# Kernel tuning notes

Hardware: AMD Instinct MI355X
Metric: run time of the kernel (lower is better)

The kernel has to match this reference:

```python
import jax, jax.numpy as jnp
import numpy as np

B, S = 32, 8192
HE, HD = 256, 256  # encoder_hidden_size, decoder_hidden_size


def setup_inputs() -> dict:
    key = jax.random.key(0)
    ks = jax.random.split(key, 8)
    scale = 1.0 / np.sqrt(HD)
    scale_e = 1.0 / np.sqrt(HE)
    return {
        "query": jax.random.normal(ks[0], (B, 1, HD), dtype=jnp.float32),
        "keys": jax.random.normal(ks[1], (B, S, HE), dtype=jnp.float32),
        "Wa_w": jax.random.uniform(ks[2], (HD, HD), jnp.float32, -scale, scale),
        "Wa_b": jax.random.uniform(ks[3], (HD,), jnp.float32, -scale, scale),
        "Ua_w": jax.random.uniform(ks[4], (HD, HE), jnp.float32, -scale_e, scale_e),
        "Ua_b": jax.random.uniform(ks[5], (HD,), jnp.float32, -scale_e, scale_e),
        "Va_w": jax.random.uniform(ks[6], (1, HD), jnp.float32, -scale, scale),
        "Va_b": jax.random.uniform(ks[7], (1,), jnp.float32, -scale, scale),
    }


def reference(query, keys, Wa_w, Wa_b, Ua_w, Ua_b, Va_w, Va_b):
    # q_proj: [B, 1, HD]; k_proj: [B, S, HD]
    q_proj = jnp.einsum("bqd,hd->bqh", query, Wa_w) + Wa_b
    k_proj = jnp.einsum("bse,he->bsh", keys, Ua_w) + Ua_b
    # scores: [B, S] -> [B, 1, S]
    scores = jnp.einsum("bsh,h->bs", jnp.tanh(q_proj + k_proj), Va_w[0]) + Va_b[0]
    weights = jax.nn.softmax(scores, axis=-1)[:, None, :]  # [B, 1, S]
    context = jnp.einsum("bqs,bse->bqe", weights, keys)    # [B, 1, HE]
    return (context, weights)
```

## Files before the change

kernel.cpp:

```cpp
#include <hip/hip_runtime.h>
#include <hip/hip_bf16.h>
#include <stdint.h>

#define B_ 32
#define S_ 8192
#define HD_ 256
#define HE_ 256
#define CHUNK 256
#define ROWS 16
#define MSTEPS (CHUNK/ROWS)
#define NCHUNK (S_/CHUNK)

typedef __attribute__((ext_vector_type(8))) short bf16x8;
typedef __attribute__((ext_vector_type(4))) float f32x4;

__device__ __forceinline__ uint32_t cvt_pk_bf16(float lo, float hi) {
  uint32_t r;
  asm("v_cvt_pk_bf16_f32 %0, %1, %2" : "=v"(r) : "v"(lo), "v"(hi));
  return r;
}
__device__ __forceinline__ float bf2f(unsigned short h) {
  return __uint_as_float(((uint32_t)h) << 16);
}
__device__ __forceinline__ float tanh_fast(float x) {
  float e = __expf(2.0f * x);
  return 1.0f - 2.0f * __builtin_amdgcn_rcpf(e + 1.0f);
}
template<int CTRL>
__device__ __forceinline__ float dpp_shr_add(float v) {
  int t = __builtin_amdgcn_update_dpp(0, __float_as_int(v), CTRL, 0xf, 0xf, true);
  return v + __int_as_float(t);
}
__device__ __forceinline__ float row16_sum(float v) {
  v = dpp_shr_add<0x118>(v);
  v = dpp_shr_add<0x114>(v);
  v = dpp_shr_add<0x112>(v);
  v = dpp_shr_add<0x111>(v);
  return v;
}

__global__ void prep_kernel(const float* __restrict__ query,
                            const float* __restrict__ Wa_w,
                            const float* __restrict__ Wa_b,
                            const float* __restrict__ Ua_w,
                            const float* __restrict__ Ua_b,
                            float* __restrict__ qv,
                            unsigned short* __restrict__ ua_bf) {
  const int blk = blockIdx.x, t = threadIdx.x;
  if (blk < B_) {
    __shared__ float qs[HD_];
    qs[t] = query[blk * HD_ + t];
    __syncthreads();
    const float* wr = Wa_w + (size_t)t * HD_;
    float s = Wa_b[t] + Ua_b[t];
#pragma unroll 8
    for (int d = 0; d < HD_; ++d) s += qs[d] * wr[d];
    qv[blk * HD_ + t] = s;
  } else {
    const int base = (blk - B_) * 2048 + t * 8;
    float4 v0 = *(const float4*)(Ua_w + base);
    float4 v1 = *(const float4*)(Ua_w + base + 4);
    uint4 pk;
    pk.x = cvt_pk_bf16(v0.x, v0.y);
    pk.y = cvt_pk_bf16(v0.z, v0.w);
    pk.z = cvt_pk_bf16(v1.x, v1.y);
    pk.w = cvt_pk_bf16(v1.z, v1.w);
    *(uint4*)(ua_bf + base) = pk;
  }
}

__global__ __launch_bounds__(512)
__attribute__((amdgpu_waves_per_eu(4, 4)))
void main_kernel(const float* __restrict__ keys,
                 const float* __restrict__ qv,
                 const float* __restrict__ Va_w,
                 const unsigned short* __restrict__ ua_bf,
                 float* __restrict__ wexp_g,
                 float* __restrict__ partials) {
  __shared__ __align__(16) char kt[2 * ROWS * 512];
  __shared__ float sc[ROWS][9];
  __shared__ float swp[ROWS];
  __shared__ float num2[512];

  const int t = threadIdx.x;
  const int b = blockIdx.y;
  const int chunk = blockIdx.x;
  const int s0 = chunk * CHUNK;
  const int lane = t & 63;
  const int w = t >> 6;
  const int ln = lane & 15;
  const int hi = lane >> 4;

  const unsigned short* ub0 = ua_bf + (size_t)(w * 32 + ln) * HE_ + hi * 8;
  const unsigned short* ub1 = ub0 + 16 * HE_;
  bf16x8 bb0[8], bb1[8];
#pragma unroll
  for (int k = 0; k < 8; ++k) {
    bb0[k] = *(const bf16x8*)(ub0 + k * 32);
    bb1[k] = *(const bf16x8*)(ub1 + k * 32);
  }
  const float q0  = qv[b * HD_ + w * 32 + ln];
  const float q1  = qv[b * HD_ + w * 32 + 16 + ln];
  const float va0 = Va_w[w * 32 + ln];
  const float va1 = Va_w[w * 32 + 16 + ln];

  const int srow = t >> 5;
  const int scch = t & 31;
  const float* ksrc = keys + ((size_t)b * S_ + s0 + srow) * HE_ + scch * 8;
  const int ldsoff = srow * 512 + ((scch * 16) ^ ((srow & 7) << 4));

  {
    float4 a0 = *(const float4*)(ksrc);
    float4 a1 = *(const float4*)(ksrc + 4);
    uint4 pk;
    pk.x = cvt_pk_bf16(a0.x, a0.y);
    pk.y = cvt_pk_bf16(a0.z, a0.w);
    pk.z = cvt_pk_bf16(a1.x, a1.y);
    pk.w = cvt_pk_bf16(a1.z, a1.w);
    *(uint4*)(kt + ldsoff) = pk;
  }
  __syncthreads();

  const int half = t >> 8;
  const int e2 = (t & 255) * 2;
  const int asw = (ln & 7) << 4;
  float num = 0.f;

  for (int i = 0; i < MSTEPS; ++i) {
    char* cur = kt + (i & 1) * (ROWS * 512);
    char* nxt = kt + ((i + 1) & 1) * (ROWS * 512);

    float4 ga0, ga1;
    if (i + 1 < MSTEPS) {
      const float* kA = ksrc + (size_t)(i + 1) * ROWS * HE_;
      ga0 = *(const float4*)(kA);
      ga1 = *(const float4*)(kA + 4);
    }

    f32x4 a00 = {0.f,0.f,0.f,0.f}, a01 = {0.f,0.f,0.f,0.f};
    const char* arow = cur + ln * 512;
#pragma unroll
    for (int k = 0; k < 8; ++k) {
      bf16x8 af = *(const bf16x8*)(arow + ((k * 64 + hi * 16) ^ asw));
      a00 = __builtin_amdgcn_mfma_f32_16x16x32_bf16(af, bb0[k], a00, 0, 0, 0);
      a01 = __builtin_amdgcn_mfma_f32_16x16x32_bf16(af, bb1[k], a01, 0, 0, 0);
    }

#pragma unroll
    for (int r = 0; r < 4; ++r) {
      float v = tanh_fast(a00[r] + q0) * va0 + tanh_fast(a01[r] + q1) * va1;
      v = row16_sum(v);
      if (ln == 15) sc[hi * 4 + r][w] = v;
    }
    __syncthreads();

    if (t < ROWS) {
      float s = sc[t][0];
#pragma unroll
      for (int ww = 1; ww < 8; ++ww) s += sc[t][ww];
      float e = __expf(s);
      swp[t] = e;
      wexp_g[(size_t)b * S_ + s0 + i * ROWS + t] = e;
    }
    __syncthreads();

#pragma unroll
    for (int rr = 0; rr < 8; ++rr) {
      const int row = half * 8 + rr;
      unsigned short kv = *(const unsigned short*)(cur + row * 512 + (e2 ^ ((row & 7) << 4)));
      num += swp[row] * bf2f(kv);
    }

    if (i + 1 < MSTEPS) {
      uint4 pk;
      pk.x = cvt_pk_bf16(ga0.x, ga0.y);
      pk.y = cvt_pk_bf16(ga0.z, ga0.w);
      pk.z = cvt_pk_bf16(ga1.x, ga1.y);
      pk.w = cvt_pk_bf16(ga1.z, ga1.w);
      *(uint4*)(nxt + ldsoff) = pk;
    }
    __syncthreads();
  }

  num2[t] = num;
  __syncthreads();
  if (t < 256) {
    partials[((size_t)b * NCHUNK + chunk) * 256 + t] = num2[t] + num2[t + 256];
  }
}

__global__ void combine_kernel(const float* __restrict__ wexp_g,
                               const float* __restrict__ partials,
                               float* __restrict__ out) {
  __shared__ float red[4];
  __shared__ float rdsh;
  const int b = blockIdx.x, t = threadIdx.x;
  const float* we = wexp_g + (size_t)b * S_;
  float s = 0.f;
#pragma unroll 4
  for (int i = t; i < S_; i += 256) s += we[i];
#pragma unroll
  for (int mm = 32; mm; mm >>= 1) s += __shfl_xor(s, mm, 64);
  if ((t & 63) == 0) red[t >> 6] = s;
  __syncthreads();
  if (t == 0) rdsh = 1.0f / (red[0] + red[1] + red[2] + red[3]);
  __syncthreads();
  const float rd = rdsh;

  const float* pb = partials + (size_t)b * NCHUNK * 256;
  float num = 0.f;
#pragma unroll 4
  for (int i = 0; i < NCHUNK; ++i) num += pb[i * 256 + t];
  out[b * HE_ + t] = num * rd;

  float* wout = out + B_ * HE_ + (size_t)b * S_;
#pragma unroll 4
  for (int i = t; i < S_; i += 256) wout[i] = we[i] * rd;
}

extern "C" void kernel_launch(void* const* d_in, const int* in_sizes, int n_in,
                              void* d_out, int out_size, void* d_ws, size_t ws_size,
                              hipStream_t stream) {
  const float* query = (const float*)d_in[0];
  const float* keys  = (const float*)d_in[1];
  const float* Wa_w  = (const float*)d_in[2];
  const float* Wa_b  = (const float*)d_in[3];
  const float* Ua_w  = (const float*)d_in[4];
  const float* Ua_b  = (const float*)d_in[5];
  const float* Va_w  = (const float*)d_in[6];
  float* out = (float*)d_out;

  char* ws = (char*)d_ws;
  float* qv             = (float*)ws;
  unsigned short* ua_bf = (unsigned short*)(ws + 32 * 1024);
  float* wexp_g         = (float*)(ws + 160 * 1024);
  float* partials       = (float*)(ws + 160 * 1024 + 1048576);

  prep_kernel<<<64, 256, 0, stream>>>(query, Wa_w, Wa_b, Ua_w, Ua_b, qv, ua_bf);
  dim3 g(NCHUNK, B_);
  main_kernel<<<g, 512, 0, stream>>>(keys, qv, Va_w, ua_bf, wexp_g, partials);
  combine_kernel<<<B_, 256, 0, stream>>>(wexp_g, partials, out);
}
```

Before: 89.07 us.

## Remove per-step barrier via LDS atomic score reduction and per-wave row ownership

Each wave now adds its partial row score straight into a double-buffered LDS accumulator with atomicAdd, replacing the per-wave score table and the single-thread reduction. This removes one __syncthreads per inner step, since every wave then reads the summed scores and computes the exponentials itself. The weighted key accumulation is reorganised so that each wave owns two rows and each lane handles four consecutive elements through a 64-bit LDS read, and a final cross-wave reduction follows. In exchange the exp is computed redundantly in every lane, LDS atomics are introduced, and float summation order becomes nondeterministic.

```diff
diff --git a/kernel.cpp b/kernel.cpp
--- a/kernel.cpp
+++ b/kernel.cpp
@@ -78,9 +78,8 @@
                  float* __restrict__ wexp_g,
                  float* __restrict__ partials) {
   __shared__ __align__(16) char kt[2 * ROWS * 512];
-  __shared__ float sc[ROWS][9];
-  __shared__ float swp[ROWS];
-  __shared__ float num2[512];
+  __shared__ float sc_sum[2][16];
+  __shared__ __align__(16) float num_l[8][64][4];
 
   const int t = threadIdx.x;
   const int b = blockIdx.y;
@@ -109,6 +108,7 @@
   const float* ksrc = keys + ((size_t)b * S_ + s0 + srow) * HE_ + scch * 8;
   const int ldsoff = srow * 512 + ((scch * 16) ^ ((srow & 7) << 4));
 
+  if (t < 32) ((float*)sc_sum)[t] = 0.f;
   {
     float4 a0 = *(const float4*)(ksrc);
     float4 a1 = *(const float4*)(ksrc + 4);
@@ -121,10 +121,9 @@
   }
   __syncthreads();
 
-  const int half = t >> 8;
-  const int e2 = (t & 255) * 2;
   const int asw = (ln & 7) << 4;
-  float num = 0.f;
+  const int nsw = (w & 7) << 4;
+  float num4[4] = {0.f, 0.f, 0.f, 0.f};
 
   for (int i = 0; i < MSTEPS; ++i) {
     char* cur = kt + (i & 1) * (ROWS * 512);
@@ -150,25 +149,26 @@
     for (int r = 0; r < 4; ++r) {
       float v = tanh_fast(a00[r] + q0) * va0 + tanh_fast(a01[r] + q1) * va1;
       v = row16_sum(v);
-      if (ln == 15) sc[hi * 4 + r][w] = v;
+      if (ln == 15) atomicAdd(&sc_sum[i & 1][hi * 4 + r], v);
     }
     __syncthreads();
 
-    if (t < ROWS) {
-      float s = sc[t][0];
-#pragma unroll
-      for (int ww = 1; ww < 8; ++ww) s += sc[t][ww];
-      float e = __expf(s);
-      swp[t] = e;
-      wexp_g[(size_t)b * S_ + s0 + i * ROWS + t] = e;
-    }
-    __syncthreads();
-
-#pragma unroll
-    for (int rr = 0; rr < 8; ++rr) {
-      const int row = half * 8 + rr;
-      unsigned short kv = *(const unsigned short*)(cur + row * 512 + (e2 ^ ((row & 7) << 4)));
-      num += swp[row] * bf2f(kv);
+    const float e0 = __expf(sc_sum[i & 1][w]);
+    const float e8 = __expf(sc_sum[i & 1][w + 8]);
+    if (lane == 0) {
+      float* wg = wexp_g + (size_t)b * S_ + s0 + i * ROWS;
+      wg[w] = e0;
+      wg[w + 8] = e8;
+    }
+    if (t < 16) sc_sum[(i + 1) & 1][t] = 0.f;
+
+    {
+      uint2 kv0 = *(const uint2*)(cur + w * 512 + ((lane * 8) ^ nsw));
+      uint2 kv1 = *(const uint2*)(cur + (w + 8) * 512 + ((lane * 8) ^ nsw));
+      num4[0] += e0 * bf2f((unsigned short)(kv0.x & 0xffff)) + e8 * bf2f((unsigned short)(kv1.x & 0xffff));
+      num4[1] += e0 * bf2f((unsigned short)(kv0.x >> 16))    + e8 * bf2f((unsigned short)(kv1.x >> 16));
+      num4[2] += e0 * bf2f((unsigned short)(kv0.y & 0xffff)) + e8 * bf2f((unsigned short)(kv1.y & 0xffff));
+      num4[3] += e0 * bf2f((unsigned short)(kv0.y >> 16))    + e8 * bf2f((unsigned short)(kv1.y >> 16));
     }
 
     if (i + 1 < MSTEPS) {
@@ -182,10 +182,13 @@
     __syncthreads();
   }
 
-  num2[t] = num;
+  *(float4*)&num_l[w][lane][0] = make_float4(num4[0], num4[1], num4[2], num4[3]);
   __syncthreads();
   if (t < 256) {
-    partials[((size_t)b * NCHUNK + chunk) * 256 + t] = num2[t] + num2[t + 256];
+    float s = 0.f;
+#pragma unroll
+    for (int ww = 0; ww < 8; ++ww) s += num_l[ww][t >> 2][t & 3];
+    partials[((size_t)b * NCHUNK + chunk) * 256 + t] = s;
   }
 }
 
```

Measured after the change: 85.00 us. 4.6% less time.
